# Kernel optimization log

Hardware: AMD Instinct MI355X
Metric: run time of the kernel (lower is better)

Reference implementation:

```python
import jax, jax.numpy as jnp
import numpy as np

H, NH, HD = 1024, 16, 64
B, T, S = 2, 1024, 3
NOISE, STEP, TEMP, NSTEPS = 0.1, 0.01, 1.0, 5
LN_EPS = 1e-5


def setup_inputs() -> dict:
    key = jax.random.key(0)
    ks = jax.random.split(key, 9)
    return {
        "queries": jax.random.normal(ks[0], (B, NH, T, HD), jnp.float32),
        "keys": jax.random.normal(ks[1], (B, NH, T, HD), jnp.float32),
        "values": jax.random.normal(ks[2], (B, NH, T, HD), jnp.float32),
        "hidden_states": jax.random.normal(ks[3], (B, T, H), jnp.float32),
        "W1": jax.random.normal(ks[4], (H, H), jnp.float32) * 0.02,
        "b1": jnp.zeros((H,), jnp.float32),
        "ln_g": jnp.ones((H,), jnp.float32),
        "ln_b": jnp.zeros((H,), jnp.float32),
        "W2": jax.random.normal(ks[5], (H, H), jnp.float32) * 0.02,
        "b2": jnp.zeros((H,), jnp.float32),
        "hyp_noise": jax.random.normal(ks[6], (S, B, NH, T, HD), jnp.float32),
        "ref_noise": jax.random.normal(ks[7], (S, NSTEPS - 1, B, NH, T, HD), jnp.float32),
    }


def _attention_energy(q, k, v):
    # q: [S,B,H,T,D]; k,v: [B,H,T,D] -> energy [S,B]
    scores = jnp.einsum('sbhtd,bhud->sbhtu', q, k) / jnp.sqrt(jnp.float32(q.shape[-1]))
    attn = jax.nn.softmax(scores, axis=-1)
    out = jnp.einsum('sbhtu,bhud->sbhtd', attn, v)
    out_mag = jnp.linalg.norm(out, axis=-1).mean(axis=(2, 3))          # [S,B]
    entropy = -(attn * jnp.log(attn + 1e-8)).sum(axis=-1).mean(axis=(2, 3))
    align = (q * k[None]).sum(axis=-1).mean(axis=(2, 3))
    return out_mag - 0.1 * entropy - 0.05 * align


def reference(queries, keys, values, hidden_states, W1, b1, ln_g, ln_b, W2, b2,
              hyp_noise, ref_noise):
    # query_predictor: Linear -> LayerNorm -> ReLU -> Linear
    x = hidden_states @ W1.T + b1
    mu = x.mean(axis=-1, keepdims=True)
    var = ((x - mu) ** 2).mean(axis=-1, keepdims=True)
    x = (x - mu) / jnp.sqrt(var + LN_EPS) * ln_g + ln_b
    x = jax.nn.relu(x)
    ctx = x @ W2.T + b2                                   # [B,T,H]
    ctx = ctx.reshape(B, T, NH, HD).transpose(0, 2, 1, 3) # [B,NH,T,HD]

    # exploration hypotheses, refined jointly over the sample axis
    q = queries[None] + hyp_noise * NOISE                 # [S,B,NH,T,HD]
    for step in range(NSTEPS):
        q = q - STEP * (q - ctx[None])                    # PCN prediction-error update
        if step < NSTEPS - 1:
            q = q + ref_noise[:, step] * 0.01

    energies = _attention_energy(q, keys, values)         # [S,B]
    probs = jax.nn.softmax(-energies / TEMP, axis=0)      # [S,B]
    selected = jnp.einsum('sb,sbhtd->bhtd', probs, q)     # softmax-weighted mix
    return selected, keys, values
```

## Files before the change

### kernel.cpp

```cpp
#include <hip/hip_runtime.h>
#include <hip/hip_bf16.h>
#include <math.h>

#define NB 2
#define NHH 16
#define TT 1024
#define HDD 64
#define NSS 3
#define HH 1024
#define MMR 2048

typedef float f4 __attribute__((ext_vector_type(4)));
typedef short bf16x8 __attribute__((ext_vector_type(8)));
typedef unsigned short u16;
typedef u16 u16x4 __attribute__((ext_vector_type(4)));

__device__ inline u16 f2bf(float f) {
    union { float f; unsigned u; } v; v.f = f;
    unsigned r = (v.u + 0x7FFFu + ((v.u >> 16) & 1u)) >> 16;
    return (u16)r;
}
__device__ inline float bf2f(u16 u) {
    union { unsigned u; float f; } v; v.u = ((unsigned)u) << 16;
    return v.f;
}

__device__ inline float red16sum(float v) {
    v += __shfl_xor(v, 1);
    v += __shfl_xor(v, 2);
    v += __shfl_xor(v, 4);
    v += __shfl_xor(v, 8);
    return v;
}
__device__ inline float red64sum(float v) {
    v += __shfl_xor(v, 1);
    v += __shfl_xor(v, 2);
    v += __shfl_xor(v, 4);
    v += __shfl_xor(v, 8);
    v += __shfl_xor(v, 16);
    v += __shfl_xor(v, 32);
    return v;
}

__global__ __launch_bounds__(256) void k_cvt4(const float* __restrict__ s0, u16* __restrict__ d0,
                                              const float* __restrict__ s1, u16* __restrict__ d1,
                                              const float* __restrict__ s2, u16* __restrict__ d2,
                                              const float* __restrict__ s3, u16* __restrict__ d3,
                                              float* __restrict__ outk) {
    int b = blockIdx.x;
    if (b >= 4096) {
        int i = (b - 4096) * 256 + threadIdx.x;
        f4 v = ((const f4*)s3)[i];
        ((f4*)outk)[i] = v;
        u16x4 o;
        o[0] = f2bf(v[0] * 0.125f); o[1] = f2bf(v[1] * 0.125f);
        o[2] = f2bf(v[2] * 0.125f); o[3] = f2bf(v[3] * 0.125f);
        ((u16x4*)d3)[i] = o;
        return;
    }
    const float* s; u16* d; int base;
    if (b < 2048)      { s = s0; d = d0; base = 0; }
    else if (b < 3072) { s = s1; d = d1; base = 2048; }
    else               { s = s2; d = d2; base = 3072; }
    int i = (b - base) * 256 + threadIdx.x;
    f4 v = ((const f4*)s)[i];
    u16x4 o;
    o[0] = f2bf(v[0]); o[1] = f2bf(v[1]); o[2] = f2bf(v[2]); o[3] = f2bf(v[3]);
    ((u16x4*)d)[i] = o;
}

__global__ __launch_bounds__(256) void k_vtrans(const float* __restrict__ V,
                                                u16* __restrict__ Vt,
                                                float* __restrict__ outv) {
    __shared__ float tile[64][65];
    int bh = blockIdx.y, t0 = blockIdx.x * 64;
    int r = threadIdx.x >> 2, c0 = (threadIdx.x & 3) * 16;
    const float* vp = V + ((size_t)bh * TT + t0) * HDD;
#pragma unroll
    for (int j = 0; j < 16; j += 4) {
        f4 v = *(const f4*)(vp + r * HDD + c0 + j);
        tile[r][c0 + j + 0] = v[0]; tile[r][c0 + j + 1] = v[1];
        tile[r][c0 + j + 2] = v[2]; tile[r][c0 + j + 3] = v[3];
        *(f4*)(outv + ((size_t)bh * TT + t0 + r) * HDD + c0 + j) = v;
    }
    __syncthreads();
    int d = threadIdx.x >> 2, x0 = (threadIdx.x & 3) * 16;
    u16* op = Vt + ((size_t)bh * HDD + d) * TT + t0 + x0;
#pragma unroll
    for (int j = 0; j < 16; j += 4) {
        u16x4 o;
        o[0] = f2bf(tile[x0 + j + 0][d]); o[1] = f2bf(tile[x0 + j + 1][d]);
        o[2] = f2bf(tile[x0 + j + 2][d]); o[3] = f2bf(tile[x0 + j + 3][d]);
        *(u16x4*)(op + j) = o;
    }
}

template <int EPI>
__global__ __launch_bounds__(256) void k_gemm_bt(const u16* __restrict__ A,
                                                 const u16* __restrict__ Bm,
                                                 const float* __restrict__ bias,
                                                 float* __restrict__ out) {
    const int K = 1024, N = 1024;
    int w = threadIdx.x >> 6, l = threadIdx.x & 63, lr = l & 15, lg = l >> 4;
    int m0 = blockIdx.y * 64 + w * 16;
    int n0 = blockIdx.x * 64;
    const u16* ap = A + (size_t)(m0 + lr) * K + lg * 8;
    const u16* bp = Bm + (size_t)(n0 + lr) * K + lg * 8;
    f4 z4 = {0.f, 0.f, 0.f, 0.f};
    f4 acc[4] = {z4, z4, z4, z4};
#pragma unroll 2
    for (int kk = 0; kk < K; kk += 32) {
        bf16x8 a  = *(const bf16x8*)(ap + kk);
        bf16x8 b0 = *(const bf16x8*)(bp + kk);
        bf16x8 b1 = *(const bf16x8*)(bp + 16 * K + kk);
        bf16x8 b2 = *(const bf16x8*)(bp + 32 * K + kk);
        bf16x8 b3 = *(const bf16x8*)(bp + 48 * K + kk);
        acc[0] = __builtin_amdgcn_mfma_f32_16x16x32_bf16(a, b0, acc[0], 0, 0, 0);
        acc[1] = __builtin_amdgcn_mfma_f32_16x16x32_bf16(a, b1, acc[1], 0, 0, 0);
        acc[2] = __builtin_amdgcn_mfma_f32_16x16x32_bf16(a, b2, acc[2], 0, 0, 0);
        acc[3] = __builtin_amdgcn_mfma_f32_16x16x32_bf16(a, b3, acc[3], 0, 0, 0);
    }
#pragma unroll
    for (int cf = 0; cf < 4; ++cf) {
        int col = n0 + cf * 16 + lr;
        float bs = bias[col];
#pragma unroll
        for (int r = 0; r < 4; ++r) {
            int row = m0 + lg * 4 + r;
            float v = acc[cf][r] + bs;
            if (EPI == 0) {
                out[(size_t)row * N + col] = v;
            } else {
                int b = row >> 10, t = row & 1023, nh = col >> 6, hd = col & 63;
                out[(((size_t)(b * NHH + nh)) * TT + t) * HDD + hd] = v;
            }
        }
    }
}

__global__ __launch_bounds__(256) void k_lnrelu(const float* __restrict__ X,
                                                const float* __restrict__ g,
                                                const float* __restrict__ bta,
                                                u16* __restrict__ xr) {
    int row = blockIdx.x;
    f4 v = ((const f4*)(X + (size_t)row * HH))[threadIdx.x];
    float s = v[0] + v[1] + v[2] + v[3];
    float s2 = v[0] * v[0] + v[1] * v[1] + v[2] * v[2] + v[3] * v[3];
    s = red64sum(s);
    s2 = red64sum(s2);
    __shared__ float red[8];
    int w = threadIdx.x >> 6, l = threadIdx.x & 63;
    if (l == 0) { red[w] = s; red[w + 4] = s2; }
    __syncthreads();
    float S1 = red[0] + red[1] + red[2] + red[3];
    float S2 = red[4] + red[5] + red[6] + red[7];
    float mu = S1 * (1.0f / 1024.0f);
    float var = S2 * (1.0f / 1024.0f) - mu * mu;
    float rstd = rsqrtf(var + 1e-5f);
    f4 gv = ((const f4*)g)[threadIdx.x];
    f4 bv = ((const f4*)bta)[threadIdx.x];
    u16x4 o;
#pragma unroll
    for (int j = 0; j < 4; ++j) {
        float y = (v[j] - mu) * rstd * gv[j] + bv[j];
        y = fmaxf(y, 0.f);
        o[j] = f2bf(y);
    }
    ((u16x4*)(xr + (size_t)row * HH))[threadIdx.x] = o;
}

__global__ __launch_bounds__(256, 3) void k_attn(const float* __restrict__ que,
                                                 const float* __restrict__ ctx,
                                                 const float* __restrict__ hyp,
                                                 const float* __restrict__ rn,
                                                 const u16* __restrict__ Kb,
                                                 const u16* __restrict__ Vt,
                                                 u16* __restrict__ qq,
                                                 float* __restrict__ part) {
    int bi = blockIdx.x;
    int qt2 = bi & 7, h = (bi >> 3) & 15, sb = bi >> 7;
    int s = sb >> 1, b = sb & 1;
    int bh = b * NHH + h;
    int w = threadIdx.x >> 6, l = threadIdx.x & 63, lr = l & 15, lg = l >> 4;
    int b4 = (l >> 4) & 1, b5 = (l >> 5) & 1;
    int t0 = qt2 * 128;
    f4 z4 = {0.f, 0.f, 0.f, 0.f};

    __shared__ u16 Ks[4096];
    __shared__ u16 Vs[4096];

    const float A5 = 0.9509900499f, CC = 1.0f - A5, CH = 0.1f * A5;
    const float C0 = 0.0096059601f, C1 = 0.0097029900f, C2 = 0.0098010000f, C3 = 0.0099f;
    const float* quep = que + ((size_t)bh * TT) * HDD;
    const float* ctxp = ctx + ((size_t)bh * TT) * HDD;
    const float* hypp = hyp + ((size_t)(sb * NHH + h) * TT) * HDD;
    const float* rn0p = rn + ((size_t)(((s * 4 + 0) * 2 + b) * NHH + h) * TT) * HDD;
    const float* rn1p = rn + ((size_t)(((s * 4 + 1) * 2 + b) * NHH + h) * TT) * HDD;
    const float* rn2p = rn + ((size_t)(((s * 4 + 2) * 2 + b) * NHH + h) * TT) * HDD;
    const float* rn3p = rn + ((size_t)(((s * 4 + 3) * 2 + b) * NHH + h) * TT) * HDD;
    u16* qqp = qq + ((size_t)(sb * NHH + h) * TT) * HDD;

    bf16x8 aq[2][2];
#pragma unroll
    for (int qr = 0; qr < 2; ++qr) {
        size_t ro = (size_t)(t0 + w * 32 + qr * 16 + lr) * HDD;
#pragma unroll
        for (int c = 0; c < 2; ++c) {
            int d0 = c * 32 + lg * 8;
            f4 va, vb;
#pragma unroll
            for (int half = 0; half < 2; ++half) {
                size_t off = ro + d0 + half * 4;
                f4 v = A5 * *(const f4*)(quep + off);
                v += CC * *(const f4*)(ctxp + off);
                v += CH * __builtin_nontemporal_load((const f4*)(hypp + off));
                v += C0 * __builtin_nontemporal_load((const f4*)(rn0p + off));
                v += C1 * __builtin_nontemporal_load((const f4*)(rn1p + off));
                v += C2 * __builtin_nontemporal_load((const f4*)(rn2p + off));
                v += C3 * __builtin_nontemporal_load((const f4*)(rn3p + off));
                if (half == 0) va = v; else vb = v;
            }
            union { bf16x8 f; u16 u[8]; int4 i4; } o;
#pragma unroll
            for (int j = 0; j < 4; ++j) { o.u[j] = f2bf(va[j]); o.u[4 + j] = f2bf(vb[j]); }
            aq[qr][c] = o.f;
            *(int4*)(qqp + ro + d0) = o.i4;
        }
    }

    const u16* kbase = Kb + (size_t)bh * TT * HDD;
    const u16* vbase = Vt + (size_t)bh * HDD * TT;
    int u0 = threadIdx.x, u1 = threadIdx.x + 256;
    const u16* kg0 = kbase + u0 * 8;
    const u16* kg1 = kbase + u1 * 8;
    const u16* vg0 = vbase + (size_t)(u0 >> 3) * TT + (u0 & 7) * 8;
    const u16* vg1 = vbase + (size_t)(u1 >> 3) * TT + (u1 & 7) * 8;
    int ko0 = (u0 >> 3) * 128 + (((u0 & 7) ^ ((u0 >> 3) & 7)) << 4);
    int ko1 = (u1 >> 3) * 128 + (((u1 & 7) ^ ((u1 >> 3) & 7)) << 4);
    char* KsB = (char*)Ks;
    char* VsB = (char*)Vs;

    int4 kr0 = *(const int4*)(kg0);
    int4 kr1 = *(const int4*)(kg1);
    int4 vr0 = *(const int4*)(vg0);
    int4 vr1 = *(const int4*)(vg1);

    f4 acco[2][4] = {{z4, z4, z4, z4}, {z4, z4, z4, z4}};
    float zacc[2] = {0.f, 0.f};
    float wacc[2] = {0.f, 0.f};

    for (int kt = 0; kt < 16; ++kt) {
        __syncthreads();
        *(int4*)(KsB + ko0) = kr0;
        *(int4*)(KsB + ko1) = kr1;
        *(int4*)(VsB + ko0) = vr0;
        *(int4*)(VsB + ko1) = vr1;
        if (kt < 15) {
            kr0 = *(const int4*)(kg0 + (kt + 1) * 4096);
            kr1 = *(const int4*)(kg1 + (kt + 1) * 4096);
            vr0 = *(const int4*)(vg0 + (kt + 1) * 64);
            vr1 = *(const int4*)(vg1 + (kt + 1) * 64);
        }
        __syncthreads();

        f4 st[2][4];
#pragma unroll
        for (int cf = 0; cf < 4; ++cf) {
            int row = cf * 16 + lr, rs = row & 7;
            bf16x8 bk0 = *(const bf16x8*)(KsB + row * 128 + ((lg ^ rs) << 4));
            bf16x8 bk1 = *(const bf16x8*)(KsB + row * 128 + (((4 + lg) ^ rs) << 4));
            f4 t0a = __builtin_amdgcn_mfma_f32_16x16x32_bf16(bk0, aq[0][0], z4, 0, 0, 0);
            st[0][cf] = __builtin_amdgcn_mfma_f32_16x16x32_bf16(bk1, aq[0][1], t0a, 0, 0, 0);
            f4 t1a = __builtin_amdgcn_mfma_f32_16x16x32_bf16(bk0, aq[1][0], z4, 0, 0, 0);
            st[1][cf] = __builtin_amdgcn_mfma_f32_16x16x32_bf16(bk1, aq[1][1], t1a, 0, 0, 0);
        }

        bf16x8 pa[2][2];
#pragma unroll
        for (int qr = 0; qr < 2; ++qr) {
            unsigned pk[4][2];
            float zp = 0.f, wp = 0.f;
#pragma unroll
            for (int cf = 0; cf < 4; ++cf) {
                float p0 = __expf(st[qr][cf][0]);
                float p1 = __expf(st[qr][cf][1]);
                float p2 = __expf(st[qr][cf][2]);
                float p3 = __expf(st[qr][cf][3]);
                zp += (p0 + p1) + (p2 + p3);
                wp = fmaf(p0, st[qr][cf][0], wp);
                wp = fmaf(p1, st[qr][cf][1], wp);
                wp = fmaf(p2, st[qr][cf][2], wp);
                wp = fmaf(p3, st[qr][cf][3], wp);
                asm("v_cvt_pk_bf16_f32 %0, %1, %2" : "=v"(pk[cf][0]) : "v"(p0), "v"(p1));
                asm("v_cvt_pk_bf16_f32 %0, %1, %2" : "=v"(pk[cf][1]) : "v"(p2), "v"(p3));
            }
            zacc[qr] += zp;
            wacc[qr] += wp;
            unsigned keep0[2][2], got0[2][2];
#pragma unroll
            for (int ch = 0; ch < 2; ++ch)
#pragma unroll
                for (int wi = 0; wi < 2; ++wi) {
                    unsigned own  = b5 ? pk[2 * ch + 1][wi] : pk[2 * ch][wi];
                    unsigned send = b5 ? pk[2 * ch][wi]     : pk[2 * ch + 1][wi];
                    keep0[ch][wi] = own;
                    got0[ch][wi]  = (unsigned)__shfl_xor((int)send, 32);
                }
            union { unsigned u[4]; bf16x8 f; } pc[2];
#pragma unroll
            for (int ch = 0; ch < 2; ++ch)
#pragma unroll
                for (int wi = 0; wi < 2; ++wi) {
                    unsigned own2  = (b5 == b4) ? keep0[ch][wi] : got0[ch][wi];
                    unsigned send2 = (b5 == b4) ? got0[ch][wi]  : keep0[ch][wi];
                    unsigned got2  = (unsigned)__shfl_xor((int)send2, 16);
                    pc[ch].u[wi]     = b4 ? got2 : own2;
                    pc[ch].u[2 + wi] = b4 ? own2 : got2;
                }
            pa[qr][0] = pc[0].f;
            pa[qr][1] = pc[1].f;
        }

#pragma unroll
        for (int cf = 0; cf < 4; ++cf) {
            int row = cf * 16 + lr, rs = row & 7;
            bf16x8 bv0 = *(const bf16x8*)(VsB + row * 128 + ((lg ^ rs) << 4));
            bf16x8 bv1 = *(const bf16x8*)(VsB + row * 128 + (((4 + lg) ^ rs) << 4));
            acco[0][cf] = __builtin_amdgcn_mfma_f32_16x16x32_bf16(pa[0][0], bv0, acco[0][cf], 0, 0, 0);
            acco[0][cf] = __builtin_amdgcn_mfma_f32_16x16x32_bf16(pa[0][1], bv1, acco[0][cf], 0, 0, 0);
            acco[1][cf] = __builtin_amdgcn_mfma_f32_16x16x32_bf16(pa[1][0], bv0, acco[1][cf], 0, 0, 0);
            acco[1][cf] = __builtin_amdgcn_mfma_f32_16x16x32_bf16(pa[1][1], bv1, acco[1][cf], 0, 0, 0);
        }
    }

    float mag_lane = 0.f, ent_lane = 0.f;
#pragma unroll
    for (int qr = 0; qr < 2; ++qr) {
        float zf = zacc[qr];
        zf += __shfl_xor(zf, 16); zf += __shfl_xor(zf, 32);
        float wf = wacc[qr];
        wf += __shfl_xor(wf, 16); wf += __shfl_xor(wf, 32);
        ent_lane += __logf(zf) - wf / zf;
#pragma unroll
        for (int r = 0; r < 4; ++r) {
            float ssq = acco[qr][0][r] * acco[qr][0][r] + acco[qr][1][r] * acco[qr][1][r] +
                        acco[qr][2][r] * acco[qr][2][r] + acco[qr][3][r] * acco[qr][3][r];
            ssq = red16sum(ssq);
            float zq = __shfl(zf, lg * 4 + r);
            mag_lane += sqrtf(ssq) / zq;
        }
    }
    float magw = red64sum(mag_lane) * (1.0f / 16.0f);
    float entw = red64sum(ent_lane) * 0.25f;

    int arow = threadIdx.x >> 1, ah = (threadIdx.x & 1) * 32;
    const u16* qa = qqp + (size_t)(t0 + arow) * HDD + ah;
    const u16* ka = Kb + (((size_t)bh) * TT + t0 + arow) * HDD + ah;
    float al = 0.f;
#pragma unroll
    for (int j = 0; j < 32; j += 4) {
        u16x4 qv4 = *(const u16x4*)(qa + j);
        u16x4 kv4 = *(const u16x4*)(ka + j);
        al += bf2f(qv4[0]) * bf2f(kv4[0]) + bf2f(qv4[1]) * bf2f(kv4[1]) +
              bf2f(qv4[2]) * bf2f(kv4[2]) + bf2f(qv4[3]) * bf2f(kv4[3]);
    }
    al = red64sum(al) * 8.0f;

    __shared__ float red[4][3];
    if (l == 0) { red[w][0] = magw; red[w][1] = entw; red[w][2] = al; }
    __syncthreads();
    if (threadIdx.x == 0) {
        part[bi * 3 + 0] = red[0][0] + red[1][0] + red[2][0] + red[3][0];
        part[bi * 3 + 1] = red[0][1] + red[1][1] + red[2][1] + red[3][1];
        part[bi * 3 + 2] = red[0][2] + red[1][2] + red[2][2] + red[3][2];
    }
}

__global__ void k_finalize(const float* __restrict__ part, float* __restrict__ probs) {
    int w = threadIdx.x >> 6, l = threadIdx.x & 63;
    __shared__ float eng[6];
    if (w < 6) {
        float a0 = 0.f, a1 = 0.f, a2 = 0.f;
        for (int i = l; i < 128; i += 64) {
            const float* pp = part + (size_t)(w * 128 + i) * 3;
            a0 += pp[0]; a1 += pp[1]; a2 += pp[2];
        }
        a0 = red64sum(a0); a1 = red64sum(a1); a2 = red64sum(a2);
        if (l == 0) {
            const float inv = 1.0f / 16384.0f;
            eng[w] = a0 * inv - 0.1f * (a1 * inv) - 0.05f * (a2 * inv);
        }
    }
    __syncthreads();
    if (threadIdx.x < 2) {
        int b = threadIdx.x;
        float e0 = -eng[0 + b], e1 = -eng[2 + b], e2 = -eng[4 + b];
        float mx = fmaxf(e0, fmaxf(e1, e2));
        float x0 = __expf(e0 - mx), x1 = __expf(e1 - mx), x2 = __expf(e2 - mx);
        float inv = 1.0f / (x0 + x1 + x2);
        probs[0 + b] = x0 * inv;
        probs[2 + b] = x1 * inv;
        probs[4 + b] = x2 * inv;
    }
}

__global__ __launch_bounds__(256) void k_select(const u16* __restrict__ qq,
                                                const float* __restrict__ probs,
                                                float* __restrict__ out) {
    const int NQ4 = 524288;
    int i = blockIdx.x * 256 + threadIdx.x;
    int b = i >> 18;
    float p0 = probs[0 + b], p1 = probs[2 + b], p2 = probs[4 + b];
    u16x4 a0 = ((const u16x4*)qq)[i];
    u16x4 a1 = ((const u16x4*)qq)[NQ4 + i];
    u16x4 a2 = ((const u16x4*)qq)[2 * NQ4 + i];
    f4 v;
#pragma unroll
    for (int j = 0; j < 4; ++j)
        v[j] = p0 * bf2f(a0[j]) + p1 * bf2f(a1[j]) + p2 * bf2f(a2[j]);
    ((f4*)out)[i] = v;
}

extern "C" void kernel_launch(void* const* d_in, const int* in_sizes, int n_in,
                              void* d_out, int out_size, void* d_ws, size_t ws_size,
                              hipStream_t stream) {
    const float* queries = (const float*)d_in[0];
    const float* keys    = (const float*)d_in[1];
    const float* values  = (const float*)d_in[2];
    const float* hs      = (const float*)d_in[3];
    const float* W1      = (const float*)d_in[4];
    const float* b1      = (const float*)d_in[5];
    const float* ln_g    = (const float*)d_in[6];
    const float* ln_b    = (const float*)d_in[7];
    const float* W2      = (const float*)d_in[8];
    const float* b2      = (const float*)d_in[9];
    const float* hyp     = (const float*)d_in[10];
    const float* rn      = (const float*)d_in[11];
    float* out = (float*)d_out;
    char* ws = (char*)d_ws;

    const size_t MB = 1024ull * 1024ull;
    u16*   qq16 = (u16*)(ws);
    u16*   hs_b = (u16*)(ws + 0 * MB);
    u16*   w1_b = (u16*)(ws + 4 * MB);
    u16*   w2_b = (u16*)(ws + 6 * MB);
    float* X    = (float*)(ws + 8 * MB);
    u16*   xr   = (u16*)(ws + 16 * MB);
    float* ctx  = (float*)(ws + 24 * MB);
    u16*   k_b  = (u16*)(ws + 32 * MB);
    u16*   vt_b = (u16*)(ws + 36 * MB);
    float* part = (float*)(ws + 40 * MB);
    float* probs= (float*)(ws + 40 * MB + 65536);

    k_cvt4<<<6144, 256, 0, stream>>>(hs, hs_b, W1, w1_b, W2, w2_b, keys, k_b,
                                     out + 2097152);
    k_vtrans<<<dim3(16, 32), 256, 0, stream>>>(values, vt_b, out + 4194304);

    k_gemm_bt<0><<<dim3(16, 32), 256, 0, stream>>>(hs_b, w1_b, b1, X);
    k_lnrelu<<<2048, 256, 0, stream>>>(X, ln_g, ln_b, xr);
    k_gemm_bt<1><<<dim3(16, 32), 256, 0, stream>>>(xr, w2_b, b2, ctx);

    k_attn<<<768, 256, 0, stream>>>(queries, ctx, hyp, rn, k_b, vt_b, qq16, part);
    k_finalize<<<1, 384, 0, stream>>>(part, probs);
    k_select<<<2048, 256, 0, stream>>>(qq16, probs, out);
}
```

Baseline: 183.3 us.

## Fold query/ctx blend into GEMM epilogue and halve attention tile per block

The A5*queries + CC*ctx blend moves into the second GEMM's epilogue, so the attention kernel reads one precomputed base tensor instead of two. The attention kernel now handles 64 query rows per block instead of 128, doubling the grid to 1536 blocks and raising the occupancy hint from 3 to 6. Blocks are reordered so heads vary fastest. The alignment term is taken from the diagonal of the score tile instead of a separate reload of q and K. The cost is that each block re-streams K/V tiles for fewer queries, doubling K/V traffic through LDS and L2.

```diff
diff --git a/kernel.cpp b/kernel.cpp
--- a/kernel.cpp
+++ b/kernel.cpp
@@ -99,6 +99,7 @@
 __global__ __launch_bounds__(256) void k_gemm_bt(const u16* __restrict__ A,
                                                  const u16* __restrict__ Bm,
                                                  const float* __restrict__ bias,
+                                                 const float* __restrict__ que,
                                                  float* __restrict__ out) {
     const int K = 1024, N = 1024;
     int w = threadIdx.x >> 6, l = threadIdx.x & 63, lr = l & 15, lg = l >> 4;
@@ -120,6 +121,7 @@
         acc[2] = __builtin_amdgcn_mfma_f32_16x16x32_bf16(a, b2, acc[2], 0, 0, 0);
         acc[3] = __builtin_amdgcn_mfma_f32_16x16x32_bf16(a, b3, acc[3], 0, 0, 0);
     }
+    const float A5 = 0.9509900499f, CC = 1.0f - A5;
 #pragma unroll
     for (int cf = 0; cf < 4; ++cf) {
         int col = n0 + cf * 16 + lr;
@@ -132,7 +134,8 @@
                 out[(size_t)row * N + col] = v;
             } else {
                 int b = row >> 10, t = row & 1023, nh = col >> 6, hd = col & 63;
-                out[(((size_t)(b * NHH + nh)) * TT + t) * HDD + hd] = v;
+                size_t oidx = (((size_t)(b * NHH + nh)) * TT + t) * HDD + hd;
+                out[oidx] = A5 * que[oidx] + CC * v;
             }
         }
     }
@@ -169,8 +172,7 @@
     ((u16x4*)(xr + (size_t)row * HH))[threadIdx.x] = o;
 }
 
-__global__ __launch_bounds__(256, 3) void k_attn(const float* __restrict__ que,
-                                                 const float* __restrict__ ctx,
+__global__ __launch_bounds__(256, 6) void k_attn(const float* __restrict__ basep_,
                                                  const float* __restrict__ hyp,
                                                  const float* __restrict__ rn,
                                                  const u16* __restrict__ Kb,
@@ -178,21 +180,23 @@
                                                  u16* __restrict__ qq,
                                                  float* __restrict__ part) {
     int bi = blockIdx.x;
-    int qt2 = bi & 7, h = (bi >> 3) & 15, sb = bi >> 7;
-    int s = sb >> 1, b = sb & 1;
+    int p_ = bi & 31, j_ = bi >> 5;
+    int h = p_ & 15, b = p_ >> 4;
+    int s = j_ >> 4, qt = j_ & 15;
+    int sb = s * 2 + b;
     int bh = b * NHH + h;
+    int pi = sb * 256 + h * 16 + qt;
     int w = threadIdx.x >> 6, l = threadIdx.x & 63, lr = l & 15, lg = l >> 4;
     int b4 = (l >> 4) & 1, b5 = (l >> 5) & 1;
-    int t0 = qt2 * 128;
+    int t0 = qt * 64;
     f4 z4 = {0.f, 0.f, 0.f, 0.f};
 
     __shared__ u16 Ks[4096];
     __shared__ u16 Vs[4096];
 
-    const float A5 = 0.9509900499f, CC = 1.0f - A5, CH = 0.1f * A5;
+    const float CH = 0.1f * 0.9509900499f;
     const float C0 = 0.0096059601f, C1 = 0.0097029900f, C2 = 0.0098010000f, C3 = 0.0099f;
-    const float* quep = que + ((size_t)bh * TT) * HDD;
-    const float* ctxp = ctx + ((size_t)bh * TT) * HDD;
+    const float* basep = basep_ + ((size_t)bh * TT) * HDD;
     const float* hypp = hyp + ((size_t)(sb * NHH + h) * TT) * HDD;
     const float* rn0p = rn + ((size_t)(((s * 4 + 0) * 2 + b) * NHH + h) * TT) * HDD;
     const float* rn1p = rn + ((size_t)(((s * 4 + 1) * 2 + b) * NHH + h) * TT) * HDD;
@@ -200,10 +204,9 @@
     const float* rn3p = rn + ((size_t)(((s * 4 + 3) * 2 + b) * NHH + h) * TT) * HDD;
     u16* qqp = qq + ((size_t)(sb * NHH + h) * TT) * HDD;
 
-    bf16x8 aq[2][2];
-#pragma unroll
-    for (int qr = 0; qr < 2; ++qr) {
-        size_t ro = (size_t)(t0 + w * 32 + qr * 16 + lr) * HDD;
+    bf16x8 aq[2];
+    {
+        size_t ro = (size_t)(t0 + w * 16 + lr) * HDD;
 #pragma unroll
         for (int c = 0; c < 2; ++c) {
             int d0 = c * 32 + lg * 8;
@@ -211,8 +214,7 @@
 #pragma unroll
             for (int half = 0; half < 2; ++half) {
                 size_t off = ro + d0 + half * 4;
-                f4 v = A5 * *(const f4*)(quep + off);
-                v += CC * *(const f4*)(ctxp + off);
+                f4 v = *(const f4*)(basep + off);
                 v += CH * __builtin_nontemporal_load((const f4*)(hypp + off));
                 v += C0 * __builtin_nontemporal_load((const f4*)(rn0p + off));
                 v += C1 * __builtin_nontemporal_load((const f4*)(rn1p + off));
@@ -223,7 +225,7 @@
             union { bf16x8 f; u16 u[8]; int4 i4; } o;
 #pragma unroll
             for (int j = 0; j < 4; ++j) { o.u[j] = f2bf(va[j]); o.u[4 + j] = f2bf(vb[j]); }
-            aq[qr][c] = o.f;
+            aq[c] = o.f;
             *(int4*)(qqp + ro + d0) = o.i4;
         }
     }
@@ -245,9 +247,8 @@
     int4 vr0 = *(const int4*)(vg0);
     int4 vr1 = *(const int4*)(vg1);
 
-    f4 acco[2][4] = {{z4, z4, z4, z4}, {z4, z4, z4, z4}};
-    float zacc[2] = {0.f, 0.f};
-    float wacc[2] = {0.f, 0.f};
+    f4 acco[4] = {z4, z4, z4, z4};
+    float zacc = 0.f, wacc = 0.f, al_lane = 0.f;
 
     for (int kt = 0; kt < 16; ++kt) {
         __syncthreads();
@@ -263,39 +264,43 @@
         }
         __syncthreads();
 
-        f4 st[2][4];
+        f4 st[4];
 #pragma unroll
         for (int cf = 0; cf < 4; ++cf) {
             int row = cf * 16 + lr, rs = row & 7;
             bf16x8 bk0 = *(const bf16x8*)(KsB + row * 128 + ((lg ^ rs) << 4));
             bf16x8 bk1 = *(const bf16x8*)(KsB + row * 128 + (((4 + lg) ^ rs) << 4));
-            f4 t0a = __builtin_amdgcn_mfma_f32_16x16x32_bf16(bk0, aq[0][0], z4, 0, 0, 0);
-            st[0][cf] = __builtin_amdgcn_mfma_f32_16x16x32_bf16(bk1, aq[0][1], t0a, 0, 0, 0);
-            f4 t1a = __builtin_amdgcn_mfma_f32_16x16x32_bf16(bk0, aq[1][0], z4, 0, 0, 0);
-            st[1][cf] = __builtin_amdgcn_mfma_f32_16x16x32_bf16(bk1, aq[1][1], t1a, 0, 0, 0);
-        }
-
-        bf16x8 pa[2][2];
-#pragma unroll
-        for (int qr = 0; qr < 2; ++qr) {
+            f4 t0a = __builtin_amdgcn_mfma_f32_16x16x32_bf16(bk0, aq[0], z4, 0, 0, 0);
+            st[cf] = __builtin_amdgcn_mfma_f32_16x16x32_bf16(bk1, aq[1], t0a, 0, 0, 0);
+        }
+
+        if (kt == qt) {
+            f4 stw = w == 0 ? st[0] : (w == 1 ? st[1] : (w == 2 ? st[2] : st[3]));
+            int rr = lr & 3;
+            float dsel = rr == 0 ? stw[0] : (rr == 1 ? stw[1] : (rr == 2 ? stw[2] : stw[3]));
+            if (lg == (lr >> 2)) al_lane += dsel * 8.0f;
+        }
+
+        bf16x8 pa[2];
+        {
             unsigned pk[4][2];
             float zp = 0.f, wp = 0.f;
 #pragma unroll
             for (int cf = 0; cf < 4; ++cf) {
-                float p0 = __expf(st[qr][cf][0]);
-                float p1 = __expf(st[qr][cf][1]);
-                float p2 = __expf(st[qr][cf][2]);
-                float p3 = __expf(st[qr][cf][3]);
+                float p0 = __expf(st[cf][0]);
+                float p1 = __expf(st[cf][1]);
+                float p2 = __expf(st[cf][2]);
+                float p3 = __expf(st[cf][3]);
                 zp += (p0 + p1) + (p2 + p3);
-                wp = fmaf(p0, st[qr][cf][0], wp);
-                wp = fmaf(p1, st[qr][cf][1], wp);
-                wp = fmaf(p2, st[qr][cf][2], wp);
-                wp = fmaf(p3, st[qr][cf][3], wp);
+                wp = fmaf(p0, st[cf][0], wp);
+                wp = fmaf(p1, st[cf][1], wp);
+                wp = fmaf(p2, st[cf][2], wp);
+                wp = fmaf(p3, st[cf][3], wp);
                 asm("v_cvt_pk_bf16_f32 %0, %1, %2" : "=v"(pk[cf][0]) : "v"(p0), "v"(p1));
                 asm("v_cvt_pk_bf16_f32 %0, %1, %2" : "=v"(pk[cf][1]) : "v"(p2), "v"(p3));
             }
-            zacc[qr] += zp;
-            wacc[qr] += wp;
+            zacc += zp;
+            wacc += wp;
             unsigned keep0[2][2], got0[2][2];
 #pragma unroll
             for (int ch = 0; ch < 2; ++ch)
@@ -317,8 +322,8 @@
                     pc[ch].u[wi]     = b4 ? got2 : own2;
                     pc[ch].u[2 + wi] = b4 ? own2 : got2;
                 }
-            pa[qr][0] = pc[0].f;
-            pa[qr][1] = pc[1].f;
+            pa[0] = pc[0].f;
+            pa[1] = pc[1].f;
         }
 
 #pragma unroll
@@ -326,53 +331,36 @@
             int row = cf * 16 + lr, rs = row & 7;
             bf16x8 bv0 = *(const bf16x8*)(VsB + row * 128 + ((lg ^ rs) << 4));
             bf16x8 bv1 = *(const bf16x8*)(VsB + row * 128 + (((4 + lg) ^ rs) << 4));
-            acco[0][cf] = __builtin_amdgcn_mfma_f32_16x16x32_bf16(pa[0][0], bv0, acco[0][cf], 0, 0, 0);
-            acco[0][cf] = __builtin_amdgcn_mfma_f32_16x16x32_bf16(pa[0][1], bv1, acco[0][cf], 0, 0, 0);
-            acco[1][cf] = __builtin_amdgcn_mfma_f32_16x16x32_bf16(pa[1][0], bv0, acco[1][cf], 0, 0, 0);
-            acco[1][cf] = __builtin_amdgcn_mfma_f32_16x16x32_bf16(pa[1][1], bv1, acco[1][cf], 0, 0, 0);
-        }
-    }
-
-    float mag_lane = 0.f, ent_lane = 0.f;
-#pragma unroll
-    for (int qr = 0; qr < 2; ++qr) {
-        float zf = zacc[qr];
-        zf += __shfl_xor(zf, 16); zf += __shfl_xor(zf, 32);
-        float wf = wacc[qr];
-        wf += __shfl_xor(wf, 16); wf += __shfl_xor(wf, 32);
-        ent_lane += __logf(zf) - wf / zf;
-#pragma unroll
-        for (int r = 0; r < 4; ++r) {
-            float ssq = acco[qr][0][r] * acco[qr][0][r] + acco[qr][1][r] * acco[qr][1][r] +
-                        acco[qr][2][r] * acco[qr][2][r] + acco[qr][3][r] * acco[qr][3][r];
-            ssq = red16sum(ssq);
-            float zq = __shfl(zf, lg * 4 + r);
-            mag_lane += sqrtf(ssq) / zq;
-        }
+            acco[cf] = __builtin_amdgcn_mfma_f32_16x16x32_bf16(pa[0], bv0, acco[cf], 0, 0, 0);
+            acco[cf] = __builtin_amdgcn_mfma_f32_16x16x32_bf16(pa[1], bv1, acco[cf], 0, 0, 0);
+        }
+    }
+
+    float zf = zacc;
+    zf += __shfl_xor(zf, 16); zf += __shfl_xor(zf, 32);
+    float wf = wacc;
+    wf += __shfl_xor(wf, 16); wf += __shfl_xor(wf, 32);
+    float ent_lane = __logf(zf) - wf / zf;
+    float mag_lane = 0.f;
+#pragma unroll
+    for (int r = 0; r < 4; ++r) {
+        float ssq = acco[0][r] * acco[0][r] + acco[1][r] * acco[1][r] +
+                    acco[2][r] * acco[2][r] + acco[3][r] * acco[3][r];
+        ssq = red16sum(ssq);
+        float zq = __shfl(zf, lg * 4 + r);
+        mag_lane += sqrtf(ssq) / zq;
     }
     float magw = red64sum(mag_lane) * (1.0f / 16.0f);
     float entw = red64sum(ent_lane) * 0.25f;
-
-    int arow = threadIdx.x >> 1, ah = (threadIdx.x & 1) * 32;
-    const u16* qa = qqp + (size_t)(t0 + arow) * HDD + ah;
-    const u16* ka = Kb + (((size_t)bh) * TT + t0 + arow) * HDD + ah;
-    float al = 0.f;
-#pragma unroll
-    for (int j = 0; j < 32; j += 4) {
-        u16x4 qv4 = *(const u16x4*)(qa + j);
-        u16x4 kv4 = *(const u16x4*)(ka + j);
-        al += bf2f(qv4[0]) * bf2f(kv4[0]) + bf2f(qv4[1]) * bf2f(kv4[1]) +
-              bf2f(qv4[2]) * bf2f(kv4[2]) + bf2f(qv4[3]) * bf2f(kv4[3]);
-    }
-    al = red64sum(al) * 8.0f;
+    float al   = red64sum(al_lane);
 
     __shared__ float red[4][3];
     if (l == 0) { red[w][0] = magw; red[w][1] = entw; red[w][2] = al; }
     __syncthreads();
     if (threadIdx.x == 0) {
-        part[bi * 3 + 0] = red[0][0] + red[1][0] + red[2][0] + red[3][0];
-        part[bi * 3 + 1] = red[0][1] + red[1][1] + red[2][1] + red[3][1];
-        part[bi * 3 + 2] = red[0][2] + red[1][2] + red[2][2] + red[3][2];
+        part[pi * 3 + 0] = red[0][0] + red[1][0] + red[2][0] + red[3][0];
+        part[pi * 3 + 1] = red[0][1] + red[1][1] + red[2][1] + red[3][1];
+        part[pi * 3 + 2] = red[0][2] + red[1][2] + red[2][2] + red[3][2];
     }
 }
 
@@ -381,8 +369,8 @@
     __shared__ float eng[6];
     if (w < 6) {
         float a0 = 0.f, a1 = 0.f, a2 = 0.f;
-        for (int i = l; i < 128; i += 64) {
-            const float* pp = part + (size_t)(w * 128 + i) * 3;
+        for (int i = l; i < 256; i += 64) {
+            const float* pp = part + (size_t)(w * 256 + i) * 3;
             a0 += pp[0]; a1 += pp[1]; a2 += pp[2];
         }
         a0 = red64sum(a0); a1 = red64sum(a1); a2 = red64sum(a2);
@@ -446,7 +434,7 @@
     u16*   w2_b = (u16*)(ws + 6 * MB);
     float* X    = (float*)(ws + 8 * MB);
     u16*   xr   = (u16*)(ws + 16 * MB);
-    float* ctx  = (float*)(ws + 24 * MB);
+    float* base = (float*)(ws + 24 * MB);
     u16*   k_b  = (u16*)(ws + 32 * MB);
     u16*   vt_b = (u16*)(ws + 36 * MB);
     float* part = (float*)(ws + 40 * MB);
@@ -456,11 +444,11 @@
                                      out + 2097152);
     k_vtrans<<<dim3(16, 32), 256, 0, stream>>>(values, vt_b, out + 4194304);
 
-    k_gemm_bt<0><<<dim3(16, 32), 256, 0, stream>>>(hs_b, w1_b, b1, X);
+    k_gemm_bt<0><<<dim3(16, 32), 256, 0, stream>>>(hs_b, w1_b, b1, nullptr, X);
     k_lnrelu<<<2048, 256, 0, stream>>>(X, ln_g, ln_b, xr);
-    k_gemm_bt<1><<<dim3(16, 32), 256, 0, stream>>>(xr, w2_b, b2, ctx);
-
-    k_attn<<<768, 256, 0, stream>>>(queries, ctx, hyp, rn, k_b, vt_b, qq16, part);
+    k_gemm_bt<1><<<dim3(16, 32), 256, 0, stream>>>(xr, w2_b, b2, queries, base);
+
+    k_attn<<<1536, 256, 0, stream>>>(base, hyp, rn, k_b, vt_b, qq16, part);
     k_finalize<<<1, 384, 0, stream>>>(part, probs);
     k_select<<<2048, 256, 0, stream>>>(qq16, probs, out);
 }
```

New measurement: 193.2 us. 5.4% more time.
